# Kernel tuning notes

Hardware: AMD Instinct MI355X
Metric: run time of the kernel (lower is better)

The kernel has to match this reference:

```python
import jax, jax.numpy as jnp
import numpy as np

N, E, G = 50000, 800000, 64
IN, H, C = 128, 3, 64
HC = H * C


def _conv(x, src, dst, Wq, bq, Wk, bk, Wv, bv, Ws, bs, Wb):
    # node-level projections, then per-edge gather
    q = (x @ Wq + bq).reshape(-1, H, C)[dst]   # [E,H,C]
    k = (x @ Wk + bk).reshape(-1, H, C)[src]
    v = (x @ Wv + bv).reshape(-1, H, C)[src]
    alpha = (q * k).sum(-1) / jnp.sqrt(jnp.float32(C))  # [E,H]
    # segment softmax over incoming edges of each target node
    amax = jax.ops.segment_max(alpha, dst, num_segments=N)
    amax = jnp.where(jnp.isfinite(amax), amax, 0.0)
    ex = jnp.exp(alpha - amax[dst])
    denom = jax.ops.segment_sum(ex, dst, num_segments=N)
    a = ex / (denom[dst] + 1e-16)
    out = jax.ops.segment_sum(a[:, :, None] * v, dst, num_segments=N).reshape(-1, HC)
    # gated skip (beta=True, root_weight=True)
    r = x @ Ws + bs
    beta = jax.nn.sigmoid(jnp.concatenate([out, r, out - r], -1) @ Wb)  # [N,1]
    return beta * r + (1.0 - beta) * out


def setup_inputs() -> dict:
    key = jax.random.key(0)
    ks = jax.random.split(key, 32)
    x = jax.random.normal(ks[0], (N, IN), dtype=jnp.float32)
    edge_index = jax.random.randint(ks[1], (2, E), 0, N, dtype=jnp.int32)
    batch = jnp.sort(jax.random.randint(ks[2], (N,), 0, G, dtype=jnp.int32))
    s = 0.05
    def w(k, shape):
        return jax.random.normal(k, shape, dtype=jnp.float32) * s
    d = {"x": x, "edge_index": edge_index, "batch": batch}
    ins = [IN, HC]
    ki = 3
    for l in range(2):
        din = ins[l]
        d[f"Wq{l}"] = w(ks[ki], (din, HC)); ki += 1
        d[f"bq{l}"] = jnp.zeros((HC,), jnp.float32)
        d[f"Wk{l}"] = w(ks[ki], (din, HC)); ki += 1
        d[f"bk{l}"] = jnp.zeros((HC,), jnp.float32)
        d[f"Wv{l}"] = w(ks[ki], (din, HC)); ki += 1
        d[f"bv{l}"] = jnp.zeros((HC,), jnp.float32)
        d[f"Ws{l}"] = w(ks[ki], (din, HC)); ki += 1
        d[f"bs{l}"] = jnp.zeros((HC,), jnp.float32)
        d[f"Wb{l}"] = w(ks[ki], (3 * HC, 1)); ki += 1
    d["Wlin"] = w(ks[ki], (HC, 1)); ki += 1
    d["blin"] = jnp.zeros((1,), jnp.float32)
    return d


def reference(x, edge_index, batch,
              Wq0, bq0, Wk0, bk0, Wv0, bv0, Ws0, bs0, Wb0,
              Wq1, bq1, Wk1, bk1, Wv1, bv1, Ws1, bs1, Wb1,
              Wlin, blin):
    src, dst = edge_index[0], edge_index[1]
    h = _conv(x, src, dst, Wq0, bq0, Wk0, bk0, Wv0, bv0, Ws0, bs0, Wb0)
    h = jax.nn.elu(h)
    h = _conv(h, src, dst, Wq1, bq1, Wk1, bk1, Wv1, bv1, Ws1, bs1, Wb1)
    h = jax.nn.elu(h)
    # global mean pool over graphs
    cnt = jax.ops.segment_sum(jnp.ones((N,), jnp.float32), batch, num_segments=G)
    pooled = jax.ops.segment_sum(h, batch, num_segments=G) / jnp.maximum(cnt, 1.0)[:, None]
    logits = (pooled @ Wlin + blin).squeeze(-1)  # [G]
    return logits
```

## Files before the change

### kernel.cpp

```cpp
#include <hip/hip_runtime.h>
#include <math.h>

#define NNODES 50000
#define NEDGES 800000
#define NGRAPH 64
#define DIM_IN 128
#define HCDIM  192
#define QKVRW  768

typedef __attribute__((ext_vector_type(8))) short short8;
typedef __attribute__((ext_vector_type(4))) float f32x4;
typedef __attribute__((ext_vector_type(2))) float f32x2;

__device__ __forceinline__ unsigned short f2bf(float f){
  unsigned int u = __float_as_uint(f);
  unsigned int r = (u + 0x7fffu + ((u>>16)&1u)) >> 16;
  return (unsigned short)r;
}

__device__ __forceinline__ float4 bf4_to_f4(uint2 u){
  float4 f;
  f.x = __uint_as_float(u.x<<16);
  f.y = __uint_as_float(u.x & 0xffff0000u);
  f.z = __uint_as_float(u.y<<16);
  f.w = __uint_as_float(u.y & 0xffff0000u);
  return f;
}

__device__ __forceinline__ float4 fp8x4_to_f4(unsigned int u){
  f32x2 lo = __builtin_amdgcn_cvt_pk_f32_fp8((int)u, false);
  f32x2 hi = __builtin_amdgcn_cvt_pk_f32_fp8((int)u, true);
  float4 f; f.x=lo[0]; f.y=lo[1]; f.z=hi[0]; f.w=hi[1];
  return f;
}

__device__ __forceinline__ float wave_sum(float v){
#pragma unroll
  for(int off=32; off>0; off>>=1) v += __shfl_xor(v, off, 64);
  return v;
}

__global__ void zero_i(int* p, int n){
  int i = blockIdx.x*blockDim.x + threadIdx.x;
  if(i<n) p[i]=0;
}

__global__ void zero2_k(int* a, int* b, int n){
  int i = blockIdx.x*blockDim.x + threadIdx.x;
  if(i<n){ a[i]=0; b[i]=0; }
}

__global__ void hist_k(const int* __restrict__ dst, int* __restrict__ counts, int E){
  int e = blockIdx.x*blockDim.x + threadIdx.x;
  if(e<E) atomicAdd(&counts[dst[e]], 1);
}

__global__ void scan_partial(const int* __restrict__ counts, int* __restrict__ bsum, int N){
  __shared__ int lds[256];
  int t = threadIdx.x;
  int idx = blockIdx.x*256 + t;
  int v = (idx<N)? counts[idx] : 0;
  lds[t]=v; __syncthreads();
#pragma unroll
  for(int off=128; off>0; off>>=1){
    if(t<off) lds[t]+=lds[t+off];
    __syncthreads();
  }
  if(t==0) bsum[blockIdx.x]=lds[0];
}

__global__ void scan_bsum(int* bsum, int nb){
  __shared__ int lds[1024];
  int t=threadIdx.x;
  int v=(t<nb)?bsum[t]:0;
  lds[t]=v; __syncthreads();
  int x=v;
#pragma unroll
  for(int off=1; off<1024; off<<=1){
    int y=(t>=off)?lds[t-off]:0;
    __syncthreads();
    x+=y; lds[t]=x;
    __syncthreads();
  }
  if(t<nb) bsum[t]=x-v;
}

__global__ void scan_final(const int* __restrict__ counts, const int* __restrict__ bsum,
                           int* __restrict__ row_ptr, int N){
  __shared__ int lds[256];
  int t=threadIdx.x;
  int idx=blockIdx.x*256+t;
  int v=(idx<N)?counts[idx]:0;
  lds[t]=v; __syncthreads();
  int x=v;
#pragma unroll
  for(int off=1; off<256; off<<=1){
    int y=(t>=off)?lds[t-off]:0;
    __syncthreads();
    x+=y; lds[t]=x;
    __syncthreads();
  }
  if(idx<=N) row_ptr[idx]= bsum[blockIdx.x]+x-v;
}

__global__ void fill_k(const int* __restrict__ src, const int* __restrict__ dst,
                       const int* __restrict__ row_ptr, int* __restrict__ cursor,
                       int* __restrict__ csr_src, int E){
  int e = blockIdx.x*blockDim.x + threadIdx.x;
  if(e<E){
    int d = dst[e];
    int pos = row_ptr[d] + atomicAdd(&cursor[d], 1);
    csr_src[pos] = src[e];
  }
}

__global__ void cast_bf16(const float* __restrict__ X, unsigned short* __restrict__ Xb, int n4){
  int i = blockIdx.x*blockDim.x + threadIdx.x;
  int i4 = i*4;
  if(i4 < n4){
    float4 v = *(const float4*)(X+i4);
    ushort4 o; o.x=f2bf(v.x); o.y=f2bf(v.y); o.z=f2bf(v.z); o.w=f2bf(v.w);
    *(ushort4*)(Xb+i4) = o;
  }
}

__global__ void build_wt(const float* __restrict__ Wq, const float* __restrict__ Wk,
                         const float* __restrict__ Wv, const float* __restrict__ Ws,
                         const float* __restrict__ bq, const float* __restrict__ bk,
                         const float* __restrict__ bv, const float* __restrict__ bs,
                         unsigned short* __restrict__ Wt, float* __restrict__ bcat, int K){
  int idx = blockIdx.x*256 + threadIdx.x;
  if(idx < QKVRW*K){
    int c = idx / K, k = idx % K;
    int mat = c/HCDIM, cm = c%HCDIM;
    const float* W = (mat==0)?Wq:(mat==1)?Wk:(mat==2)?Wv:Ws;
    Wt[(size_t)c*K + k] = f2bf(W[(size_t)k*HCDIM + cm]);
  }
  if(idx < QKVRW){
    int mat = idx/HCDIM, cm = idx%HCDIM;
    const float* b = (mat==0)?bq:(mat==1)?bk:(mat==2)?bv:bs;
    bcat[idx] = b[cm];
  }
}

template<int K>
__global__ __launch_bounds__(256) void gemm_mfma(
    const unsigned short* __restrict__ Xb,
    const unsigned short* __restrict__ Wt,
    const float* __restrict__ bcat,
    unsigned short* __restrict__ QR,
    unsigned char* __restrict__ KV, int N)
{
  constexpr int CPR = K/8;
  __shared__ unsigned short As[128*K];
  __shared__ unsigned short Bs[64*K];
  const int tid = threadIdx.x;
  const int wv = tid>>6;
  const int lane = tid&63;
  const int m0  = blockIdx.x*128;
  const int cb  = blockIdx.y;
  const int mat = cb/3;
  const int nc0 = cb*64;

  constexpr int A_IT = 128*CPR/256;
#pragma unroll
  for(int it=0; it<A_IT; ++it){
    int p = it*256 + tid;
    int r = p/CPR, c = p%CPR;
    int cs = c ^ (r&7);
    int grow = m0 + r; if(grow > N-1) grow = N-1;
    const unsigned short* gp = Xb + (size_t)grow*K + cs*8;
    unsigned short* lp = As + (size_t)(it*256 + wv*64)*8;
    __builtin_amdgcn_global_load_lds(
        (const __attribute__((address_space(1))) unsigned int*)gp,
        (__attribute__((address_space(3))) unsigned int*)lp, 16, 0, 0);
  }
  constexpr int B_IT = 64*CPR/256;
#pragma unroll
  for(int it=0; it<B_IT; ++it){
    int p = it*256 + tid;
    int r = p/CPR, c = p%CPR;
    int cs = c ^ (r&7);
    const unsigned short* gp = Wt + (size_t)(nc0 + r)*K + cs*8;
    unsigned short* lp = Bs + (size_t)(it*256 + wv*64)*8;
    __builtin_amdgcn_global_load_lds(
        (const __attribute__((address_space(1))) unsigned int*)gp,
        (__attribute__((address_space(3))) unsigned int*)lp, 16, 0, 0);
  }
  __syncthreads();

  const int wr = wv>>1, wc = wv&1;
  const int lhi = lane>>4, llo = lane&15;
  f32x4 acc[4][2] = {};
#pragma unroll
  for(int kk=0; kk<K; kk+=32){
    short8 a[4], b[2];
    const int chunk = kk/8 + lhi;
#pragma unroll
    for(int i=0;i<4;++i){
      int rr = wr*64 + i*16 + llo;
      int cs = chunk ^ (rr&7);
      a[i] = *(const short8*)(As + (size_t)rr*K + cs*8);
    }
#pragma unroll
    for(int j=0;j<2;++j){
      int cc = wc*32 + j*16 + llo;
      int cs = chunk ^ (cc&7);
      b[j] = *(const short8*)(Bs + (size_t)cc*K + cs*8);
    }
#pragma unroll
    for(int i=0;i<4;++i)
#pragma unroll
      for(int j=0;j<2;++j)
        acc[i][j] = __builtin_amdgcn_mfma_f32_16x16x32_bf16(a[i], b[j], acc[i][j], 0,0,0);
  }

  const int col0 = nc0 + wc*32 + llo;
  float bias0 = bcat[col0];
  float bias1 = bcat[col0+16];
  if(mat==0 || mat==3){
    const int coff = (mat==0) ? col0 : col0-384;
#pragma unroll
    for(int i=0;i<4;++i){
#pragma unroll
      for(int r=0;r<4;++r){
        int grow = m0 + wr*64 + i*16 + lhi*4 + r;
        if(grow < N){
          size_t base = (size_t)grow*384 + coff;
          QR[base]      = f2bf(acc[i][0][r] + bias0);
          QR[base + 16] = f2bf(acc[i][1][r] + bias1);
        }
      }
    }
  } else {
#pragma unroll
    for(int i=0;i<4;++i){
#pragma unroll
      for(int r=0;r<4;++r){
        int grow = m0 + wr*64 + i*16 + lhi*4 + r;
        float v0 = acc[i][0][r] + bias0;
        float v1 = acc[i][1][r] + bias1;
        float n0 = __shfl_xor(v0, 1, 64);
        float n1 = __shfl_xor(v1, 1, 64);
        if(((llo&1)==0) && grow < N){
          int p0 = __builtin_amdgcn_cvt_pk_fp8_f32(v0, n0, 0, false);
          int p1 = __builtin_amdgcn_cvt_pk_fp8_f32(v1, n1, 0, false);
          unsigned char* kb = KV + (size_t)grow*384 + (col0-192);
          *(unsigned short*)(kb)    = (unsigned short)(p0 & 0xffff);
          *(unsigned short*)(kb+16) = (unsigned short)(p1 & 0xffff);
        }
      }
    }
  }
}

template<bool OUTBF>
__global__ __launch_bounds__(256) void attn_kernel(
  const unsigned short* __restrict__ QR,
  const unsigned char* __restrict__ KV,
  const int* __restrict__ row_ptr, const int* __restrict__ csr_src,
  const float* __restrict__ Wb, float* __restrict__ HoutF,
  unsigned short* __restrict__ HoutB, int N)
{
  const int wave = threadIdx.x>>6;
  const int lane = threadIdx.x&63;
  const int g    = lane>>4;
  const int l    = lane&15;
  const int n = blockIdx.x*4 + wave;
  if(n>=N) return;

  const unsigned short* nr = QR + (size_t)n*384 + 4*l;
  float4 q0 = bf4_to_f4(*(const uint2*)(nr));
  float4 q1 = bf4_to_f4(*(const uint2*)(nr+64));
  float4 q2 = bf4_to_f4(*(const uint2*)(nr+128));

  const int s0 = row_ptr[n];
  const int deg = row_ptr[n+1]-s0;

  float4 a0={0,0,0,0}, a1={0,0,0,0}, a2={0,0,0,0};
  float d0=0.f,d1=0.f,d2=0.f;

  int sCur = csr_src[s0 + (g<deg ? g : 0)];
  for(int base=0; base<deg; base+=4){
    const int inext = base + 4 + g;
    const int sNxt = csr_src[s0 + (inext<deg ? inext : 0)];
    const bool valid = (base + g < deg);
    const unsigned int* kv = (const unsigned int*)(KV + (size_t)sCur*384) + l;
    unsigned int ku0 = kv[0],  ku1 = kv[16], ku2 = kv[32];
    unsigned int vu0 = kv[48], vu1 = kv[64], vu2 = kv[80];
    float4 k0 = fp8x4_to_f4(ku0);
    float4 k1 = fp8x4_to_f4(ku1);
    float4 k2 = fp8x4_to_f4(ku2);
    float p0 = q0.x*k0.x+q0.y*k0.y+q0.z*k0.z+q0.w*k0.w;
    float p1 = q1.x*k1.x+q1.y*k1.y+q1.z*k1.z+q1.w*k1.w;
    float p2 = q2.x*k2.x+q2.y*k2.y+q2.z*k2.z+q2.w*k2.w;
#pragma unroll
    for(int off=1; off<16; off<<=1){
      p0 += __shfl_xor(p0, off, 64);
      p1 += __shfl_xor(p1, off, 64);
      p2 += __shfl_xor(p2, off, 64);
    }
    float e0 = valid ? __expf(0.125f*p0) : 0.f;
    float e1 = valid ? __expf(0.125f*p1) : 0.f;
    float e2 = valid ? __expf(0.125f*p2) : 0.f;
    d0 += e0; d1 += e1; d2 += e2;
    float4 v0 = fp8x4_to_f4(vu0);
    float4 v1 = fp8x4_to_f4(vu1);
    float4 v2 = fp8x4_to_f4(vu2);
    a0.x+=e0*v0.x; a0.y+=e0*v0.y; a0.z+=e0*v0.z; a0.w+=e0*v0.w;
    a1.x+=e1*v1.x; a1.y+=e1*v1.y; a1.z+=e1*v1.z; a1.w+=e1*v1.w;
    a2.x+=e2*v2.x; a2.y+=e2*v2.y; a2.z+=e2*v2.z; a2.w+=e2*v2.w;
    sCur = sNxt;
  }

#pragma unroll
  for(int off=16; off<64; off<<=1){
    a0.x+=__shfl_xor(a0.x,off,64); a0.y+=__shfl_xor(a0.y,off,64);
    a0.z+=__shfl_xor(a0.z,off,64); a0.w+=__shfl_xor(a0.w,off,64);
    a1.x+=__shfl_xor(a1.x,off,64); a1.y+=__shfl_xor(a1.y,off,64);
    a1.z+=__shfl_xor(a1.z,off,64); a1.w+=__shfl_xor(a1.w,off,64);
    a2.x+=__shfl_xor(a2.x,off,64); a2.y+=__shfl_xor(a2.y,off,64);
    a2.z+=__shfl_xor(a2.z,off,64); a2.w+=__shfl_xor(a2.w,off,64);
    d0+=__shfl_xor(d0,off,64); d1+=__shfl_xor(d1,off,64); d2+=__shfl_xor(d2,off,64);
  }
  const float id0=1.f/(d0+1e-16f), id1=1.f/(d1+1e-16f), id2=1.f/(d2+1e-16f);
  float4 o0, o1, o2;
  o0.x=a0.x*id0; o0.y=a0.y*id0; o0.z=a0.z*id0; o0.w=a0.w*id0;
  o1.x=a1.x*id1; o1.y=a1.y*id1; o1.z=a1.z*id1; o1.w=a1.w*id1;
  o2.x=a2.x*id2; o2.y=a2.y*id2; o2.z=a2.z*id2; o2.w=a2.w*id2;

  float4 r0 = bf4_to_f4(*(const uint2*)(nr+192));
  float4 r1 = bf4_to_f4(*(const uint2*)(nr+256));
  float4 r2 = bf4_to_f4(*(const uint2*)(nr+320));

  const float* wb = Wb + 4*l;
  float4 w00=*(const float4*)(wb),     w01=*(const float4*)(wb+64),  w02=*(const float4*)(wb+128);
  float4 w10=*(const float4*)(wb+192), w11=*(const float4*)(wb+256), w12=*(const float4*)(wb+320);
  float4 w20=*(const float4*)(wb+384), w21=*(const float4*)(wb+448), w22=*(const float4*)(wb+512);
  float z =
    o0.x*w00.x+o0.y*w00.y+o0.z*w00.z+o0.w*w00.w +
    o1.x*w01.x+o1.y*w01.y+o1.z*w01.z+o1.w*w01.w +
    o2.x*w02.x+o2.y*w02.y+o2.z*w02.z+o2.w*w02.w +
    r0.x*w10.x+r0.y*w10.y+r0.z*w10.z+r0.w*w10.w +
    r1.x*w11.x+r1.y*w11.y+r1.z*w11.z+r1.w*w11.w +
    r2.x*w12.x+r2.y*w12.y+r2.z*w12.z+r2.w*w12.w +
    (o0.x-r0.x)*w20.x+(o0.y-r0.y)*w20.y+(o0.z-r0.z)*w20.z+(o0.w-r0.w)*w20.w +
    (o1.x-r1.x)*w21.x+(o1.y-r1.y)*w21.y+(o1.z-r1.z)*w21.z+(o1.w-r1.w)*w21.w +
    (o2.x-r2.x)*w22.x+(o2.y-r2.y)*w22.y+(o2.z-r2.z)*w22.z+(o2.w-r2.w)*w22.w;
#pragma unroll
  for(int off=1; off<16; off<<=1) z += __shfl_xor(z, off, 64);
  const float beta = 1.f/(1.f+__expf(-z));
  float4 h0,h1,h2;
  h0.x=beta*r0.x+(1.f-beta)*o0.x; h0.y=beta*r0.y+(1.f-beta)*o0.y;
  h0.z=beta*r0.z+(1.f-beta)*o0.z; h0.w=beta*r0.w+(1.f-beta)*o0.w;
  h1.x=beta*r1.x+(1.f-beta)*o1.x; h1.y=beta*r1.y+(1.f-beta)*o1.y;
  h1.z=beta*r1.z+(1.f-beta)*o1.z; h1.w=beta*r1.w+(1.f-beta)*o1.w;
  h2.x=beta*r2.x+(1.f-beta)*o2.x; h2.y=beta*r2.y+(1.f-beta)*o2.y;
  h2.z=beta*r2.z+(1.f-beta)*o2.z; h2.w=beta*r2.w+(1.f-beta)*o2.w;
  h0.x=(h0.x>0.f)?h0.x:expm1f(h0.x); h0.y=(h0.y>0.f)?h0.y:expm1f(h0.y);
  h0.z=(h0.z>0.f)?h0.z:expm1f(h0.z); h0.w=(h0.w>0.f)?h0.w:expm1f(h0.w);
  h1.x=(h1.x>0.f)?h1.x:expm1f(h1.x); h1.y=(h1.y>0.f)?h1.y:expm1f(h1.y);
  h1.z=(h1.z>0.f)?h1.z:expm1f(h1.z); h1.w=(h1.w>0.f)?h1.w:expm1f(h1.w);
  h2.x=(h2.x>0.f)?h2.x:expm1f(h2.x); h2.y=(h2.y>0.f)?h2.y:expm1f(h2.y);
  h2.z=(h2.z>0.f)?h2.z:expm1f(h2.z); h2.w=(h2.w>0.f)?h2.w:expm1f(h2.w);
  if(g==0){
    if(OUTBF){
      unsigned short* hb = HoutB + (size_t)n*HCDIM + 4*l;
      ushort4 u0, u1, u2;
      u0.x=f2bf(h0.x); u0.y=f2bf(h0.y); u0.z=f2bf(h0.z); u0.w=f2bf(h0.w);
      u1.x=f2bf(h1.x); u1.y=f2bf(h1.y); u1.z=f2bf(h1.z); u1.w=f2bf(h1.w);
      u2.x=f2bf(h2.x); u2.y=f2bf(h2.y); u2.z=f2bf(h2.z); u2.w=f2bf(h2.w);
      *(ushort4*)(hb)     = u0;
      *(ushort4*)(hb+64)  = u1;
      *(ushort4*)(hb+128) = u2;
    } else {
      float* ho = HoutF + (size_t)n*HCDIM + 4*l;
      *(float4*)(ho)     = h0;
      *(float4*)(ho+64)  = h1;
      *(float4*)(ho+128) = h2;
    }
  }
}

__global__ void zero_pool(float* pooled, int* cnt){
  int i = blockIdx.x*256 + threadIdx.x;
  if(i < NGRAPH*HCDIM) ((int*)pooled)[i]=0;
  if(i < NGRAPH) cnt[i]=0;
}

__global__ void cnt_k(const int* __restrict__ batch, int* __restrict__ cnt, int N){
  __shared__ int h[NGRAPH];
  const int t = threadIdx.x;
  if(t<NGRAPH) h[t]=0;
  __syncthreads();
  int i = blockIdx.x*blockDim.x + t;
  if(i<N) atomicAdd(&h[batch[i]], 1);
  __syncthreads();
  if(t<NGRAPH && h[t]) atomicAdd(&cnt[t], h[t]);
}

__global__ void pool_k(const float* __restrict__ H, const int* __restrict__ batch,
                       float* __restrict__ pooled, int N){
  const int t = threadIdx.x;
  int start = blockIdx.x*256;
  int end = min(start+256, N);
  if(start>=N) return;
  int cur = batch[start];
  float acc = 0.f;
  for(int nn=start; nn<end; ++nn){
    int g = batch[nn];
    if(g!=cur){ atomicAdd(&pooled[(size_t)cur*HCDIM+t], acc); acc=0.f; cur=g; }
    acc += H[(size_t)nn*HCDIM+t];
  }
  atomicAdd(&pooled[(size_t)cur*HCDIM+t], acc);
}

__global__ void logits_k(const float* __restrict__ pooled, const int* __restrict__ cnt,
                         const float* __restrict__ Wlin, const float* __restrict__ blin,
                         float* __restrict__ out){
  const int g = blockIdx.x;
  const int lane = threadIdx.x;
  float c = fmaxf((float)cnt[g], 1.f);
  float s = 0.f;
#pragma unroll
  for(int j=0;j<3;++j){
    int col = j*64+lane;
    s += pooled[(size_t)g*HCDIM+col]/c * Wlin[col];
  }
  s = wave_sum(s);
  if(lane==0) out[g] = s + blin[0];
}

extern "C" void kernel_launch(void* const* d_in, const int* in_sizes, int n_in,
                              void* d_out, int out_size, void* d_ws, size_t ws_size,
                              hipStream_t stream)
{
  const int N=NNODES, E=NEDGES;
  const float* x     = (const float*)d_in[0];
  const int*   ei    = (const int*)d_in[1];
  const int*   batch = (const int*)d_in[2];
  const int* esrc = ei;
  const int* edst = ei + E;
  const float* Wq0=(const float*)d_in[3];  const float* bq0=(const float*)d_in[4];
  const float* Wk0=(const float*)d_in[5];  const float* bk0=(const float*)d_in[6];
  const float* Wv0=(const float*)d_in[7];  const float* bv0=(const float*)d_in[8];
  const float* Ws0=(const float*)d_in[9];  const float* bs0=(const float*)d_in[10];
  const float* Wb0=(const float*)d_in[11];
  const float* Wq1=(const float*)d_in[12]; const float* bq1=(const float*)d_in[13];
  const float* Wk1=(const float*)d_in[14]; const float* bk1=(const float*)d_in[15];
  const float* Wv1=(const float*)d_in[16]; const float* bv1=(const float*)d_in[17];
  const float* Ws1=(const float*)d_in[18]; const float* bs1=(const float*)d_in[19];
  const float* Wb1=(const float*)d_in[20];
  const float* Wlin=(const float*)d_in[21];
  const float* blin=(const float*)d_in[22];
  float* out = (float*)d_out;

  char* p = (char*)d_ws;
  auto alloc = [&](size_t bytes)->char*{
    char* q = p; p += (bytes+255)/256*256; return q;
  };
  unsigned short* Xb   = (unsigned short*)alloc((size_t)N*HCDIM*2);
  unsigned short* QR   = (unsigned short*)alloc((size_t)N*384*2);
  unsigned char*  KV   = (unsigned char*)alloc((size_t)N*384);
  float* H1            = (float*)alloc((size_t)N*HCDIM*4);
  unsigned short* Wt   = (unsigned short*)alloc((size_t)QKVRW*HCDIM*2);
  float* bcat          = (float*)alloc(QKVRW*4);
  int* counts  = (int*)alloc((size_t)N*4);
  int* cursor  = (int*)alloc((size_t)N*4);
  int* row_ptr = (int*)alloc((size_t)(N+1)*4);
  int* csr     = (int*)alloc((size_t)E*4);
  int* bsum    = (int*)alloc(4096);
  float* pooled= (float*)alloc((size_t)NGRAPH*HCDIM*4);
  int* cnt     = (int*)alloc(256);

  const int NB = (N+255)/256;

  zero2_k<<<(N+255)/256,256,0,stream>>>(counts,cursor,N);
  hist_k<<<(E+255)/256,256,0,stream>>>(edst,counts,E);
  scan_partial<<<NB,256,0,stream>>>(counts,bsum,N);
  scan_bsum<<<1,1024,0,stream>>>(bsum,NB);
  scan_final<<<NB,256,0,stream>>>(counts,bsum,row_ptr,N);
  fill_k<<<(E+255)/256,256,0,stream>>>(esrc,edst,row_ptr,cursor,csr,E);

  dim3 ggemm((N+127)/128, 12);
  cast_bf16<<<((N*DIM_IN/4)+255)/256,256,0,stream>>>(x, Xb, N*DIM_IN);
  build_wt<<<(QKVRW*DIM_IN+255)/256,256,0,stream>>>(Wq0,Wk0,Wv0,Ws0,bq0,bk0,bv0,bs0,Wt,bcat,DIM_IN);
  gemm_mfma<DIM_IN><<<ggemm,256,0,stream>>>(Xb,Wt,bcat,QR,KV,N);
  attn_kernel<true><<<(N+3)/4,256,0,stream>>>(QR,KV,row_ptr,csr,Wb0,nullptr,Xb,N);
  build_wt<<<(QKVRW*HCDIM+255)/256,256,0,stream>>>(Wq1,Wk1,Wv1,Ws1,bq1,bk1,bv1,bs1,Wt,bcat,HCDIM);
  gemm_mfma<HCDIM><<<ggemm,256,0,stream>>>(Xb,Wt,bcat,QR,KV,N);
  attn_kernel<false><<<(N+3)/4,256,0,stream>>>(QR,KV,row_ptr,csr,Wb1,H1,nullptr,N);

  zero_pool<<<(NGRAPH*HCDIM+255)/256,256,0,stream>>>(pooled,cnt);
  cnt_k<<<(N+255)/256,256,0,stream>>>(batch,cnt,N);
  pool_k<<<(N+255)/256,192,0,stream>>>(H1,batch,pooled,N);
  logits_k<<<NGRAPH,64,0,stream>>>(pooled,cnt,Wlin,blin,out);
}
```

Before: 432.8 us.

## Prefetch KV rows in attention, K-tile GEMM, fuse prep and count kernels

The attention loop now issues the next edge's K/V row loads before the current edge's math, deepening software pipelining of the gather. The GEMM stages K in 64-wide tiles so LDS use shrinks, which may allow more resident blocks, at the cost of extra barriers. The bf16 cast and weight-transpose kernels are merged into one launch, and the graph node count is folded into the pooling kernel to drop a launch. The prefetch raises register pressure in the attention kernel.

```diff
diff --git a/kernel.cpp b/kernel.cpp
--- a/kernel.cpp
+++ b/kernel.cpp
@@ -38,11 +38,6 @@
 #pragma unroll
   for(int off=32; off>0; off>>=1) v += __shfl_xor(v, off, 64);
   return v;
-}
-
-__global__ void zero_i(int* p, int n){
-  int i = blockIdx.x*blockDim.x + threadIdx.x;
-  if(i<n) p[i]=0;
 }
 
 __global__ void zero2_k(int* a, int* b, int n){
@@ -114,13 +109,31 @@
   }
 }
 
-__global__ void cast_bf16(const float* __restrict__ X, unsigned short* __restrict__ Xb, int n4){
-  int i = blockIdx.x*blockDim.x + threadIdx.x;
-  int i4 = i*4;
-  if(i4 < n4){
+#define CAST_BLKS (NNODES*DIM_IN/4/256)
+__global__ void prep0_k(const float* __restrict__ X, unsigned short* __restrict__ Xb,
+                        const float* __restrict__ Wq, const float* __restrict__ Wk,
+                        const float* __restrict__ Wv, const float* __restrict__ Ws,
+                        const float* __restrict__ bq, const float* __restrict__ bk,
+                        const float* __restrict__ bv, const float* __restrict__ bs,
+                        unsigned short* __restrict__ Wt, float* __restrict__ bcat){
+  if(blockIdx.x < CAST_BLKS){
+    int i4 = (blockIdx.x*256 + threadIdx.x)*4;
     float4 v = *(const float4*)(X+i4);
     ushort4 o; o.x=f2bf(v.x); o.y=f2bf(v.y); o.z=f2bf(v.z); o.w=f2bf(v.w);
     *(ushort4*)(Xb+i4) = o;
+  } else {
+    int idx = (blockIdx.x-CAST_BLKS)*256 + threadIdx.x;
+    if(idx < QKVRW*DIM_IN){
+      int c = idx / DIM_IN, k = idx % DIM_IN;
+      int mat = c/HCDIM, cm = c%HCDIM;
+      const float* W = (mat==0)?Wq:(mat==1)?Wk:(mat==2)?Wv:Ws;
+      Wt[(size_t)c*DIM_IN + k] = f2bf(W[(size_t)k*HCDIM + cm]);
+    }
+    if(idx < QKVRW){
+      int mat = idx/HCDIM, cm = idx%HCDIM;
+      const float* b = (mat==0)?bq:(mat==1)?bk:(mat==2)?bv:bs;
+      bcat[idx] = b[cm];
+    }
   }
 }
 
@@ -151,9 +164,8 @@
     unsigned short* __restrict__ QR,
     unsigned char* __restrict__ KV, int N)
 {
-  constexpr int CPR = K/8;
-  __shared__ unsigned short As[128*K];
-  __shared__ unsigned short Bs[64*K];
+  __shared__ unsigned short As[128*64];
+  __shared__ unsigned short Bs[64*64];
   const int tid = threadIdx.x;
   const int wv = tid>>6;
   const int lane = tid&63;
@@ -162,57 +174,61 @@
   const int mat = cb/3;
   const int nc0 = cb*64;
 
-  constexpr int A_IT = 128*CPR/256;
-#pragma unroll
-  for(int it=0; it<A_IT; ++it){
-    int p = it*256 + tid;
-    int r = p/CPR, c = p%CPR;
-    int cs = c ^ (r&7);
-    int grow = m0 + r; if(grow > N-1) grow = N-1;
-    const unsigned short* gp = Xb + (size_t)grow*K + cs*8;
-    unsigned short* lp = As + (size_t)(it*256 + wv*64)*8;
-    __builtin_amdgcn_global_load_lds(
-        (const __attribute__((address_space(1))) unsigned int*)gp,
-        (__attribute__((address_space(3))) unsigned int*)lp, 16, 0, 0);
-  }
-  constexpr int B_IT = 64*CPR/256;
-#pragma unroll
-  for(int it=0; it<B_IT; ++it){
-    int p = it*256 + tid;
-    int r = p/CPR, c = p%CPR;
-    int cs = c ^ (r&7);
-    const unsigned short* gp = Wt + (size_t)(nc0 + r)*K + cs*8;
-    unsigned short* lp = Bs + (size_t)(it*256 + wv*64)*8;
-    __builtin_amdgcn_global_load_lds(
-        (const __attribute__((address_space(1))) unsigned int*)gp,
-        (__attribute__((address_space(3))) unsigned int*)lp, 16, 0, 0);
-  }
-  __syncthreads();
-
   const int wr = wv>>1, wc = wv&1;
   const int lhi = lane>>4, llo = lane&15;
   f32x4 acc[4][2] = {};
-#pragma unroll
-  for(int kk=0; kk<K; kk+=32){
-    short8 a[4], b[2];
-    const int chunk = kk/8 + lhi;
-#pragma unroll
-    for(int i=0;i<4;++i){
-      int rr = wr*64 + i*16 + llo;
-      int cs = chunk ^ (rr&7);
-      a[i] = *(const short8*)(As + (size_t)rr*K + cs*8);
-    }
-#pragma unroll
-    for(int j=0;j<2;++j){
-      int cc = wc*32 + j*16 + llo;
-      int cs = chunk ^ (cc&7);
-      b[j] = *(const short8*)(Bs + (size_t)cc*K + cs*8);
-    }
-#pragma unroll
-    for(int i=0;i<4;++i)
-#pragma unroll
-      for(int j=0;j<2;++j)
-        acc[i][j] = __builtin_amdgcn_mfma_f32_16x16x32_bf16(a[i], b[j], acc[i][j], 0,0,0);
+
+  constexpr int NT = K/64;
+#pragma unroll
+  for(int kt=0; kt<NT; ++kt){
+    if(kt>0) __syncthreads();
+#pragma unroll
+    for(int it=0; it<4; ++it){
+      int p = it*256 + tid;
+      int r = p>>3, c = p&7;
+      int cs = c ^ (r&7);
+      int grow = m0 + r; if(grow > N-1) grow = N-1;
+      const unsigned short* gp = Xb + (size_t)grow*K + kt*64 + cs*8;
+      unsigned short* lp = As + (size_t)(it*256 + wv*64)*8;
+      __builtin_amdgcn_global_load_lds(
+          (const __attribute__((address_space(1))) unsigned int*)gp,
+          (__attribute__((address_space(3))) unsigned int*)lp, 16, 0, 0);
+    }
+#pragma unroll
+    for(int it=0; it<2; ++it){
+      int p = it*256 + tid;
+      int r = p>>3, c = p&7;
+      int cs = c ^ (r&7);
+      const unsigned short* gp = Wt + (size_t)(nc0 + r)*K + kt*64 + cs*8;
+      unsigned short* lp = Bs + (size_t)(it*256 + wv*64)*8;
+      __builtin_amdgcn_global_load_lds(
+          (const __attribute__((address_space(1))) unsigned int*)gp,
+          (__attribute__((address_space(3))) unsigned int*)lp, 16, 0, 0);
+    }
+    __syncthreads();
+
+#pragma unroll
+    for(int kk=0; kk<64; kk+=32){
+      short8 a[4], b[2];
+      const int chunk = (kk>>3) + lhi;
+#pragma unroll
+      for(int i=0;i<4;++i){
+        int rr = wr*64 + i*16 + llo;
+        int cs = chunk ^ (rr&7);
+        a[i] = *(const short8*)(As + rr*64 + cs*8);
+      }
+#pragma unroll
+      for(int j=0;j<2;++j){
+        int cc = wc*32 + j*16 + llo;
+        int cs = chunk ^ (cc&7);
+        b[j] = *(const short8*)(Bs + cc*64 + cs*8);
+      }
+#pragma unroll
+      for(int i=0;i<4;++i)
+#pragma unroll
+        for(int j=0;j<2;++j)
+          acc[i][j] = __builtin_amdgcn_mfma_f32_16x16x32_bf16(a[i], b[j], acc[i][j], 0,0,0);
+    }
   }
 
   const int col0 = nc0 + wc*32 + llo;
@@ -280,14 +296,21 @@
   float4 a0={0,0,0,0}, a1={0,0,0,0}, a2={0,0,0,0};
   float d0=0.f,d1=0.f,d2=0.f;
 
-  int sCur = csr_src[s0 + (g<deg ? g : 0)];
+  unsigned int ku0=0,ku1=0,ku2=0,vu0=0,vu1=0,vu2=0;
+  if(deg>0){
+    int i0 = s0 + (g<deg ? g : 0); if(i0 > NEDGES-1) i0 = NEDGES-1;
+    int sCur = csr_src[i0];
+    const unsigned int* kv = (const unsigned int*)(KV + (size_t)sCur*384) + l;
+    ku0=kv[0]; ku1=kv[16]; ku2=kv[32]; vu0=kv[48]; vu1=kv[64]; vu2=kv[80];
+  }
   for(int base=0; base<deg; base+=4){
     const int inext = base + 4 + g;
     const int sNxt = csr_src[s0 + (inext<deg ? inext : 0)];
+    const unsigned int* kvN = (const unsigned int*)(KV + (size_t)sNxt*384) + l;
+    unsigned int nk0=kvN[0], nk1=kvN[16], nk2=kvN[32];
+    unsigned int nv0=kvN[48], nv1=kvN[64], nv2=kvN[80];
+
     const bool valid = (base + g < deg);
-    const unsigned int* kv = (const unsigned int*)(KV + (size_t)sCur*384) + l;
-    unsigned int ku0 = kv[0],  ku1 = kv[16], ku2 = kv[32];
-    unsigned int vu0 = kv[48], vu1 = kv[64], vu2 = kv[80];
     float4 k0 = fp8x4_to_f4(ku0);
     float4 k1 = fp8x4_to_f4(ku1);
     float4 k2 = fp8x4_to_f4(ku2);
@@ -310,7 +333,8 @@
     a0.x+=e0*v0.x; a0.y+=e0*v0.y; a0.z+=e0*v0.z; a0.w+=e0*v0.w;
     a1.x+=e1*v1.x; a1.y+=e1*v1.y; a1.z+=e1*v1.z; a1.w+=e1*v1.w;
     a2.x+=e2*v2.x; a2.y+=e2*v2.y; a2.z+=e2*v2.z; a2.w+=e2*v2.w;
-    sCur = sNxt;
+
+    ku0=nk0; ku1=nk1; ku2=nk2; vu0=nv0; vu1=nv1; vu2=nv2;
   }
 
 #pragma unroll
@@ -388,31 +412,27 @@
   if(i < NGRAPH) cnt[i]=0;
 }
 
-__global__ void cnt_k(const int* __restrict__ batch, int* __restrict__ cnt, int N){
-  __shared__ int h[NGRAPH];
-  const int t = threadIdx.x;
-  if(t<NGRAPH) h[t]=0;
-  __syncthreads();
-  int i = blockIdx.x*blockDim.x + t;
-  if(i<N) atomicAdd(&h[batch[i]], 1);
-  __syncthreads();
-  if(t<NGRAPH && h[t]) atomicAdd(&cnt[t], h[t]);
-}
-
 __global__ void pool_k(const float* __restrict__ H, const int* __restrict__ batch,
-                       float* __restrict__ pooled, int N){
+                       float* __restrict__ pooled, int* __restrict__ cnt, int N){
   const int t = threadIdx.x;
   int start = blockIdx.x*256;
   int end = min(start+256, N);
   if(start>=N) return;
   int cur = batch[start];
   float acc = 0.f;
+  int run = 0;
   for(int nn=start; nn<end; ++nn){
     int g = batch[nn];
-    if(g!=cur){ atomicAdd(&pooled[(size_t)cur*HCDIM+t], acc); acc=0.f; cur=g; }
+    if(g!=cur){
+      atomicAdd(&pooled[(size_t)cur*HCDIM+t], acc);
+      if(t==0) atomicAdd(&cnt[cur], run);
+      acc=0.f; run=0; cur=g;
+    }
     acc += H[(size_t)nn*HCDIM+t];
+    run++;
   }
   atomicAdd(&pooled[(size_t)cur*HCDIM+t], acc);
+  if(t==0) atomicAdd(&cnt[cur], run);
 }
 
 __global__ void logits_k(const float* __restrict__ pooled, const int* __restrict__ cnt,
@@ -483,8 +503,8 @@
   fill_k<<<(E+255)/256,256,0,stream>>>(esrc,edst,row_ptr,cursor,csr,E);
 
   dim3 ggemm((N+127)/128, 12);
-  cast_bf16<<<((N*DIM_IN/4)+255)/256,256,0,stream>>>(x, Xb, N*DIM_IN);
-  build_wt<<<(QKVRW*DIM_IN+255)/256,256,0,stream>>>(Wq0,Wk0,Wv0,Ws0,bq0,bk0,bv0,bs0,Wt,bcat,DIM_IN);
+  prep0_k<<<CAST_BLKS + (QKVRW*DIM_IN+255)/256, 256, 0, stream>>>(
+      x, Xb, Wq0,Wk0,Wv0,Ws0, bq0,bk0,bv0,bs0, Wt, bcat);
   gemm_mfma<DIM_IN><<<ggemm,256,0,stream>>>(Xb,Wt,bcat,QR,KV,N);
   attn_kernel<true><<<(N+3)/4,256,0,stream>>>(QR,KV,row_ptr,csr,Wb0,nullptr,Xb,N);
   build_wt<<<(QKVRW*HCDIM+255)/256,256,0,stream>>>(Wq1,Wk1,Wv1,Ws1,bq1,bk1,bv1,bs1,Wt,bcat,HCDIM);
@@ -492,7 +512,6 @@
   attn_kernel<false><<<(N+3)/4,256,0,stream>>>(QR,KV,row_ptr,csr,Wb1,H1,nullptr,N);
 
   zero_pool<<<(NGRAPH*HCDIM+255)/256,256,0,stream>>>(pooled,cnt);
-  cnt_k<<<(N+255)/256,256,0,stream>>>(batch,cnt,N);
-  pool_k<<<(N+255)/256,192,0,stream>>>(H1,batch,pooled,N);
+  pool_k<<<(N+255)/256,192,0,stream>>>(H1,batch,pooled,cnt,N);
   logits_k<<<NGRAPH,64,0,stream>>>(pooled,cnt,Wlin,blin,out);
 }
```

After: 406.1 us. 6.2% less time.
